# Optimization experiments

Measured on AMD Instinct MI355X. Metric: run time of the kernel, lower is better.

Reference implementation:

```python
import jax, jax.numpy as jnp
import numpy as np

H = 4  # hidden size fixed by the module


def setup_inputs() -> dict:
    key = jax.random.key(0)
    ks = jax.random.split(key, 7)
    B, T, I = 4096, 1024, 8
    s_ih = 1.0 / np.sqrt(H)
    return {
        "x": jax.random.normal(ks[0], (B, T, I), dtype=jnp.float32),
        "W_ih": jax.random.uniform(ks[1], (4 * H, I), jnp.float32, -s_ih, s_ih),
        "W_hh": jax.random.uniform(ks[2], (4 * H, H), jnp.float32, -s_ih, s_ih),
        "b_ih": jax.random.uniform(ks[3], (4 * H,), jnp.float32, -s_ih, s_ih),
        "b_hh": jax.random.uniform(ks[4], (4 * H,), jnp.float32, -s_ih, s_ih),
        "fc_w": jax.random.uniform(ks[5], (1, H), jnp.float32, -0.5, 0.5),
        "fc_b": jax.random.uniform(ks[6], (1,), jnp.float32, -0.5, 0.5),
    }


def _lstm_last_hidden(x, W_ih, W_hh, b_ih, b_hh):
    B = x.shape[0]
    # Precompute input contribution for all timesteps: [B, T, 4H] -> scan over T
    xg = jnp.einsum("bti,gi->btg", x, W_ih) + (b_ih + b_hh)
    xg = jnp.swapaxes(xg, 0, 1)  # [T, B, 4H]

    def step(carry, g_t):
        h, c = carry
        gates = g_t + h @ W_hh.T  # [B, 4H]
        i, f, g, o = jnp.split(gates, 4, axis=-1)  # PyTorch gate order
        c = jax.nn.sigmoid(f) * c + jax.nn.sigmoid(i) * jnp.tanh(g)
        h = jax.nn.sigmoid(o) * jnp.tanh(c)
        return (h, c), None

    h0 = jnp.zeros((B, H), dtype=x.dtype)
    (h_last, _), _ = jax.lax.scan(step, (h0, h0), xg)
    return h_last  # [B, H]


def reference(x, W_ih, W_hh, b_ih, b_hh, fc_w, fc_b):
    h_last = _lstm_last_hidden(x, W_ih, W_hh, b_ih, b_hh)
    return h_last @ fc_w.T + fc_b  # [B, 1]
```

## Files before the change

### kernel.cpp

```cpp
#include <hip/hip_runtime.h>


#define TT 1024
#define II 8
#define CHUNK 32
#define NCHUNK (TT / CHUNK)
#define ROW (CHUNK * II)
#define SPAD 4

typedef float v2f __attribute__((ext_vector_type(2)));

template <int CTRL>
__device__ __forceinline__ float dppf(float v) {
  return __int_as_float(
      __builtin_amdgcn_mov_dpp(__float_as_int(v), CTRL, 0xF, 0xF, true));
}

__device__ __forceinline__ float fast_sigmoid(float x) {
  return __builtin_amdgcn_rcpf(1.0f + __expf(-x));
}

__device__ __forceinline__ float fast_tanh(float x) {
  return 1.0f - 2.0f * __builtin_amdgcn_rcpf(__expf(2.0f * x) + 1.0f);
}

#define GLOAD_LDS16(gp, lp)                                   \
  __builtin_amdgcn_global_load_lds(                           \
      (const __attribute__((address_space(1))) void*)(gp),    \
      (__attribute__((address_space(3))) void*)(lp), 16, 0, 0)

__global__ __launch_bounds__(128, 1) void lstm_fused(
    const float* __restrict__ x, const float* __restrict__ W_ih,
    const float* __restrict__ W_hh, const float* __restrict__ b_ih,
    const float* __restrict__ b_hh, const float* __restrict__ fc_w,
    const float* __restrict__ fc_b, float* __restrict__ out, int B) {
  const int tid = threadIdx.x;
  const int wave = tid >> 6;
  const int lane = tid & 63;
  const int j = lane & 3;
  const int grp = lane >> 2;
  const int b = blockIdx.x * 16 + grp;

  __shared__ float xs0[16][ROW + SPAD];
  __shared__ float xs1[16][ROW + SPAD];
  __shared__ float pa0[CHUNK][16][16];
  __shared__ float pa1[CHUNK][16][16];

  if (wave == 0) {
    v2f wih01[II], wih23[II];
    v2f bias01, bias23;
#pragma unroll
    for (int k = 0; k < II; ++k) {
      wih01[k] = v2f{W_ih[(0 * 4 + j) * II + k], W_ih[(1 * 4 + j) * II + k]};
      wih23[k] = v2f{W_ih[(2 * 4 + j) * II + k], W_ih[(3 * 4 + j) * II + k]};
    }
    bias01 = v2f{b_ih[0 * 4 + j] + b_hh[0 * 4 + j],
                 b_ih[1 * 4 + j] + b_hh[1 * 4 + j]};
    bias23 = v2f{b_ih[2 * 4 + j] + b_hh[2 * 4 + j],
                 b_ih[3 * 4 + j] + b_hh[3 * 4 + j]};

    const size_t blockBase = (size_t)blockIdx.x * 16;

    auto issue = [&](float(*xs)[ROW + SPAD], int t0) {
#pragma unroll
      for (int s = 0; s < 16; ++s) {
        const float* gp =
            x + (blockBase + s) * (TT * II) + (size_t)t0 * II + lane * 4;
        GLOAD_LDS16(gp, &xs[s][0]);
      }
    };

    auto produce = [&](float(*pa)[16][16], const float(*xs)[ROW + SPAD]) {
      const float* row = &xs[grp][0];
#pragma unroll 8
      for (int u = 0; u < CHUNK; ++u) {
        const float4 xa = *(const float4*)(row + u * 8);
        const float4 xb = *(const float4*)(row + u * 8 + 4);
        v2f a01 = bias01, a23 = bias23;
#define XFMA(k, val)                                    \
  {                                                     \
    v2f xv = v2f{(val), (val)};                         \
    a01 = __builtin_elementwise_fma(wih01[k], xv, a01); \
    a23 = __builtin_elementwise_fma(wih23[k], xv, a23); \
  }
        XFMA(0, xa.x) XFMA(1, xa.y) XFMA(2, xa.z) XFMA(3, xa.w)
        XFMA(4, xb.x) XFMA(5, xb.y) XFMA(6, xb.z) XFMA(7, xb.w)
#undef XFMA
        *(float4*)&pa[u][grp][j * 4] = float4{a01.x, a01.y, a23.x, a23.y};
      }
    };

    issue(xs0, 0);
    issue(xs1, CHUNK);
    produce(pa0, xs0);
    __syncthreads();

    for (int ck = 0; ck < NCHUNK; ++ck) {
      if (ck + 1 < NCHUNK)
        produce(((ck + 1) & 1) ? pa1 : pa0, ((ck + 1) & 1) ? xs1 : xs0);
      if (ck + 2 < NCHUNK) issue((ck & 1) ? xs1 : xs0, (ck + 2) * CHUNK);
      __syncthreads();
    }
  } else {
    v2f whh01[4], whh23[4];
#pragma unroll
    for (int k = 0; k < 4; ++k) {
      whh01[k] = v2f{W_hh[(0 * 4 + j) * 4 + k], W_hh[(1 * 4 + j) * 4 + k]};
      whh23[k] = v2f{W_hh[(2 * 4 + j) * 4 + k], W_hh[(3 * 4 + j) * 4 + k]};
    }
    float h = 0.0f, c = 0.0f;

    __syncthreads();

    for (int ck = 0; ck < NCHUNK; ++ck) {
      const float(*pa)[16][16] = (ck & 1) ? pa1 : pa0;
      const float* base = &pa[0][grp][j * 4];
      float4 g = *(const float4*)base;
#pragma unroll 8
      for (int u = 0; u < CHUNK; ++u) {
        const int un = (u + 1 < CHUNK) ? (u + 1) : u;
        const float4 gn = *(const float4*)(base + un * 256);

        v2f a01 = v2f{g.x, g.y};
        v2f a23 = v2f{g.z, g.w};
        const float h0 = dppf<0x00>(h);
        const float h1 = dppf<0x55>(h);
        const float h2 = dppf<0xAA>(h);
        const float h3 = dppf<0xFF>(h);
#define HFMA(k, val)                                    \
  {                                                     \
    v2f hv = v2f{(val), (val)};                         \
    a01 = __builtin_elementwise_fma(whh01[k], hv, a01); \
    a23 = __builtin_elementwise_fma(whh23[k], hv, a23); \
  }
        HFMA(0, h0) HFMA(1, h1) HFMA(2, h2) HFMA(3, h3)
#undef HFMA
        const float ig = fast_sigmoid(a01.x);
        const float fg = fast_sigmoid(a01.y);
        const float gg = fast_tanh(a23.x);
        const float og = fast_sigmoid(a23.y);
        c = fmaf(fg, c, ig * gg);
        h = og * fast_tanh(c);

        g = gn;
      }
      __syncthreads();
    }

    float v = h * fc_w[j];
    v += dppf<0xB1>(v);
    v += dppf<0x4E>(v);
    if (j == 0 && b < B) out[b] = v + fc_b[0];
  }
}

extern "C" void kernel_launch(void* const* d_in, const int* in_sizes, int n_in,
                              void* d_out, int out_size, void* d_ws,
                              size_t ws_size, hipStream_t stream) {
  const float* x = (const float*)d_in[0];
  const float* W_ih = (const float*)d_in[1];
  const float* W_hh = (const float*)d_in[2];
  const float* b_ih = (const float*)d_in[3];
  const float* b_hh = (const float*)d_in[4];
  const float* fc_w = (const float*)d_in[5];
  const float* fc_b = (const float*)d_in[6];
  float* out = (float*)d_out;

  const int B = in_sizes[0] / (TT * II);
  const int nblocks = (B + 15) / 16;
  lstm_fused<<<nblocks, 128, 0, stream>>>(x, W_ih, W_hh, b_ih, b_hh, fc_w,
                                          fc_b, out, B);
}
```

Measured before the change: 260.1 us.

## Fold log2e scaling into LSTM weights and batch-prefetch gate preactivations

Pre-scales the input and recurrent weights and biases by -log2(e) for the sigmoid gates and by 2·log2(e) for the tanh gate, so each activation becomes a bare exp2 plus rcp with no per-step multiply. The cell state is carried pre-scaled (c2 = 2·log2e·c), which removes the scaling from the tanh(c) evaluation too, and h is formed with a single fma. It also replaces the one-step-ahead LDS prefetch with double-buffered batches of 8 float4 loads, so LDS latency is hidden further ahead of the serial recurrence. The cost is higher register use and a slight change in floating-point rounding.

```diff
diff --git a/kernel.cpp b/kernel.cpp
--- a/kernel.cpp
+++ b/kernel.cpp
@@ -8,6 +8,10 @@
 #define ROW (CHUNK * II)
 #define SPAD 4
 
+#define L2E 1.4426950408889634f
+#define SIG_SCALE (-L2E)
+#define G_SCALE (2.0f * L2E)
+
 typedef float v2f __attribute__((ext_vector_type(2)));
 
 template <int CTRL>
@@ -16,12 +20,11 @@
       __builtin_amdgcn_mov_dpp(__float_as_int(v), CTRL, 0xF, 0xF, true));
 }
 
-__device__ __forceinline__ float fast_sigmoid(float x) {
-  return __builtin_amdgcn_rcpf(1.0f + __expf(-x));
+__device__ __forceinline__ float ex2(float x) {
+  return __builtin_amdgcn_exp2f(x);
 }
-
-__device__ __forceinline__ float fast_tanh(float x) {
-  return 1.0f - 2.0f * __builtin_amdgcn_rcpf(__expf(2.0f * x) + 1.0f);
+__device__ __forceinline__ float rcp(float x) {
+  return __builtin_amdgcn_rcpf(x);
 }
 
 #define GLOAD_LDS16(gp, lp)                                   \
@@ -51,13 +54,15 @@
     v2f bias01, bias23;
 #pragma unroll
     for (int k = 0; k < II; ++k) {
-      wih01[k] = v2f{W_ih[(0 * 4 + j) * II + k], W_ih[(1 * 4 + j) * II + k]};
-      wih23[k] = v2f{W_ih[(2 * 4 + j) * II + k], W_ih[(3 * 4 + j) * II + k]};
+      wih01[k] = v2f{SIG_SCALE * W_ih[(0 * 4 + j) * II + k],
+                     SIG_SCALE * W_ih[(1 * 4 + j) * II + k]};
+      wih23[k] = v2f{G_SCALE * W_ih[(2 * 4 + j) * II + k],
+                     SIG_SCALE * W_ih[(3 * 4 + j) * II + k]};
     }
-    bias01 = v2f{b_ih[0 * 4 + j] + b_hh[0 * 4 + j],
-                 b_ih[1 * 4 + j] + b_hh[1 * 4 + j]};
-    bias23 = v2f{b_ih[2 * 4 + j] + b_hh[2 * 4 + j],
-                 b_ih[3 * 4 + j] + b_hh[3 * 4 + j]};
+    bias01 = v2f{SIG_SCALE * (b_ih[0 * 4 + j] + b_hh[0 * 4 + j]),
+                 SIG_SCALE * (b_ih[1 * 4 + j] + b_hh[1 * 4 + j])};
+    bias23 = v2f{G_SCALE * (b_ih[2 * 4 + j] + b_hh[2 * 4 + j]),
+                 SIG_SCALE * (b_ih[3 * 4 + j] + b_hh[3 * 4 + j])};
 
     const size_t blockBase = (size_t)blockIdx.x * 16;
 
@@ -105,45 +110,64 @@
     v2f whh01[4], whh23[4];
 #pragma unroll
     for (int k = 0; k < 4; ++k) {
-      whh01[k] = v2f{W_hh[(0 * 4 + j) * 4 + k], W_hh[(1 * 4 + j) * 4 + k]};
-      whh23[k] = v2f{W_hh[(2 * 4 + j) * 4 + k], W_hh[(3 * 4 + j) * 4 + k]};
+      whh01[k] = v2f{SIG_SCALE * W_hh[(0 * 4 + j) * 4 + k],
+                     SIG_SCALE * W_hh[(1 * 4 + j) * 4 + k]};
+      whh23[k] = v2f{G_SCALE * W_hh[(2 * 4 + j) * 4 + k],
+                     SIG_SCALE * W_hh[(3 * 4 + j) * 4 + k]};
     }
-    float h = 0.0f, c = 0.0f;
+    float h = 0.0f, c2 = 0.0f;
+
+    auto step = [&](float4 g) {
+      const float h0 = dppf<0x00>(h);
+      const float h1 = dppf<0x55>(h);
+      const float h2 = dppf<0xAA>(h);
+      const float h3 = dppf<0xFF>(h);
+      v2f a01 = v2f{g.x, g.y};
+      v2f a23 = v2f{g.z, g.w};
+#define HFMA(k, val)                                    \
+  {                                                     \
+    v2f hv = v2f{(val), (val)};                         \
+    a01 = __builtin_elementwise_fma(whh01[k], hv, a01); \
+    a23 = __builtin_elementwise_fma(whh23[k], hv, a23); \
+  }
+      HFMA(0, h0) HFMA(1, h1) HFMA(2, h2) HFMA(3, h3)
+#undef HFMA
+      const float ig = rcp(1.0f + ex2(a01.x));
+      const float fg = rcp(1.0f + ex2(a01.y));
+      const float rg = rcp(1.0f + ex2(a23.x));
+      const float og = rcp(1.0f + ex2(a23.y));
+      const float gg2 = fmaf(rg, -2.0f * G_SCALE, G_SCALE);
+      c2 = fmaf(fg, c2, ig * gg2);
+      const float rc = rcp(1.0f + ex2(c2));
+      const float m2og = -2.0f * og;
+      h = fmaf(rc, m2og, og);
+    };
 
     __syncthreads();
 
     for (int ck = 0; ck < NCHUNK; ++ck) {
       const float(*pa)[16][16] = (ck & 1) ? pa1 : pa0;
       const float* base = &pa[0][grp][j * 4];
-      float4 g = *(const float4*)base;
-#pragma unroll 8
-      for (int u = 0; u < CHUNK; ++u) {
-        const int un = (u + 1 < CHUNK) ? (u + 1) : u;
-        const float4 gn = *(const float4*)(base + un * 256);
 
-        v2f a01 = v2f{g.x, g.y};
-        v2f a23 = v2f{g.z, g.w};
-        const float h0 = dppf<0x00>(h);
-        const float h1 = dppf<0x55>(h);
-        const float h2 = dppf<0xAA>(h);
-        const float h3 = dppf<0xFF>(h);
-#define HFMA(k, val)                                    \
-  {                                                     \
-    v2f hv = v2f{(val), (val)};                         \
-    a01 = __builtin_elementwise_fma(whh01[k], hv, a01); \
-    a23 = __builtin_elementwise_fma(whh23[k], hv, a23); \
+      float4 ra[8], rb[8];
+#define LOADB(r, u0)                                                \
+  {                                                                 \
+    _Pragma("unroll") for (int k = 0; k < 8; ++k) (r)[k] =          \
+        *(const float4*)(base + (u0 + k) * 256);                    \
   }
-        HFMA(0, h0) HFMA(1, h1) HFMA(2, h2) HFMA(3, h3)
-#undef HFMA
-        const float ig = fast_sigmoid(a01.x);
-        const float fg = fast_sigmoid(a01.y);
-        const float gg = fast_tanh(a23.x);
-        const float og = fast_sigmoid(a23.y);
-        c = fmaf(fg, c, ig * gg);
-        h = og * fast_tanh(c);
+#define COMP8(r)                                   \
+  { _Pragma("unroll") for (int k = 0; k < 8; ++k) step((r)[k]); }
 
-        g = gn;
-      }
+      LOADB(ra, 0)
+      LOADB(rb, 8)
+      COMP8(ra)
+      LOADB(ra, 16)
+      COMP8(rb)
+      LOADB(rb, 24)
+      COMP8(ra)
+      COMP8(rb)
+#undef LOADB
+#undef COMP8
       __syncthreads();
     }
 
```

Measured after the change: 259.8 us. Within noise of the previous version (-0.1%).
